# Performance work log

Measured on AMD Instinct MI355X. Metric: run time of the kernel, lower is better.

The kernel has to match this reference:

```python
import jax, jax.numpy as jnp
import numpy as np

VOL_RES = 128          # volume_res
SIGMA = 0.05           # gaussian splat sigma (normalized [0,1] coords)
SPLAT_R = 3            # splat neighborhood radius = smooth_kernel_size // 2
TET_W = 5              # tet rasterization window edge (voxels)
EPS_W = 1e-3           # weight_sum init (torch fills 0.001)

B, NV, NSURF, NF, NT = 2, 7700, 6890, 13776, 30000


def setup_inputs() -> dict:
    key = jax.random.key(0)
    k0, k1, k2, k3 = jax.random.split(key, 4)
    smpl_vertices = jax.random.uniform(k0, (B, NV, 3), dtype=jnp.float32)      # verts in [0,1]^3
    vertex_code = jax.random.uniform(k1, (B, NSURF, 3), dtype=jnp.float32)     # semantic code per surface vert
    face_indices = jax.random.randint(k2, (NF, 3), 0, NSURF, dtype=jnp.int32)
    tet_indices = jax.random.randint(k3, (NT, 4), 0, NV, dtype=jnp.int32)
    return {"smpl_vertices": smpl_vertices, "vertex_code": vertex_code,
            "face_indices": face_indices, "tet_indices": tet_indices}


def _voxelize(smpl_vertices, vertex_code, face_indices, tet_indices):
    R = VOL_RES
    R3 = R * R * R
    bsz = smpl_vertices.shape[0]

    # --- face centers / normals (computed by the torch forward; not consumed by the kernel) ---
    faces = smpl_vertices[:, face_indices]                         # (B,NF,3,3)
    face_center = faces.mean(axis=2)                               # (B,NF,3)
    v10 = faces[:, :, 0] - faces[:, :, 1]
    v12 = faces[:, :, 2] - faces[:, :, 1]
    nrm = jnp.cross(v10, v12)
    face_normal = nrm / jnp.maximum(
        jnp.linalg.norm(nrm, axis=-1, keepdims=True), 1e-5)        # F.normalize eps=1e-5
    del face_center, face_normal  # passed to the autograd fn but unused by the cuda op

    bidx = jnp.arange(bsz, dtype=jnp.int32)

    # ---------------- occupancy from tetrahedrons (point-in-tet rasterization) ----------------
    tets = smpl_vertices[:, tet_indices]                           # (B,NT,4,3)
    a = tets[:, :, 0]
    e1 = tets[:, :, 1] - a
    e2 = tets[:, :, 2] - a
    e3 = tets[:, :, 3] - a
    c23 = jnp.cross(e2, e3)
    vol6 = jnp.sum(e1 * c23, axis=-1)                              # signed 6*volume (B,NT)

    anchor = jnp.floor(jnp.min(tets, axis=2) * R).astype(jnp.int32)  # (B,NT,3) min-corner voxel
    w1 = jnp.arange(TET_W, dtype=jnp.int32)
    toff = jnp.stack(jnp.meshgrid(w1, w1, w1, indexing="ij"), -1).reshape(-1, 3)  # (W3,3) xyz
    tvox = anchor[:, :, None, :] + toff                            # (B,NT,W3,3)
    tp = (tvox.astype(jnp.float32) + 0.5) / R                      # voxel centers
    p = tp - a[:, :, None, :]                                      # (B,NT,W3,3)
    iv = 1.0 / jnp.where(jnp.abs(vol6) > 1e-12, vol6, 1.0)
    l1 = jnp.sum(p * c23[:, :, None, :], -1) * iv[:, :, None]
    l2 = jnp.sum(jnp.cross(p, e3[:, :, None, :]) * e1[:, :, None, :], -1) * iv[:, :, None]
    l3 = jnp.sum(jnp.cross(e2[:, :, None, :], p) * e1[:, :, None, :], -1) * iv[:, :, None]
    inside = (l1 >= 0) & (l2 >= 0) & (l3 >= 0) & (l1 + l2 + l3 <= 1.0)
    inside &= (jnp.abs(vol6) > 1e-12)[:, :, None]
    tvalid = jnp.all((tvox >= 0) & (tvox < R), axis=-1) & inside   # (B,NT,W3)
    # linear index, layout (b, z, y, x)
    tlin = ((bidx[:, None, None] * R + tvox[..., 2]) * R + tvox[..., 1]) * R + tvox[..., 0]
    tlin = jnp.where(tvalid, tlin, bsz * R3)                       # drop out-of-range
    occ = jnp.zeros((bsz * R3,), jnp.float32).at[tlin.reshape(-1)].max(
        tvalid.astype(jnp.float32).reshape(-1), mode="drop")

    # ---------------- gaussian semantic splat from surface vertices ----------------
    vs = smpl_vertices[:, :NSURF]                                  # (B,NS,3)
    base = jnp.floor(vs * R).astype(jnp.int32)                     # containing voxel
    o1 = jnp.arange(-SPLAT_R, SPLAT_R + 1, dtype=jnp.int32)
    offs = jnp.stack(jnp.meshgrid(o1, o1, o1, indexing="ij"), -1).reshape(-1, 3)  # (K3,3)
    svox = base[:, :, None, :] + offs                              # (B,NS,K3,3)
    ctr = (svox.astype(jnp.float32) + 0.5) / R
    d2 = jnp.sum((ctr - vs[:, :, None, :]) ** 2, axis=-1)          # (B,NS,K3)
    w = jnp.exp(-d2 / (2.0 * SIGMA * SIGMA))
    svalid = jnp.all((svox >= 0) & (svox < R), axis=-1)
    w = jnp.where(svalid, w, 0.0)
    slin = ((bidx[:, None, None] * R + svox[..., 2]) * R + svox[..., 1]) * R + svox[..., 0]
    slin = jnp.where(svalid, slin, bsz * R3).reshape(-1)

    wsum = jnp.full((bsz * R3,), EPS_W, jnp.float32).at[slin].add(w.reshape(-1), mode="drop")
    contrib = (w[..., None] * vertex_code[:, :, None, :]).reshape(-1, 3)
    sem = jnp.zeros((bsz * R3, 3), jnp.float32).at[slin].add(contrib, mode="drop")

    semantic = sem / wsum[:, None] * occ[:, None]                  # normalize + mask to body
    semantic = semantic.reshape(bsz, R, R, R, 3)                   # (B, z, y, x, C)
    return jnp.transpose(semantic, (0, 4, 1, 2, 3))                # (B, C, z, y, x)


def reference(smpl_vertices, vertex_code, face_indices, tet_indices):
    return _voxelize(smpl_vertices, vertex_code, face_indices, tet_indices)
```

## Files before the change

### kernel.cpp

```cpp
#include <hip/hip_runtime.h>
#include <math.h>

#define R 128
#define R3 (R*R*R)
#define BATCH 2
#define NV 7700
#define NSURF 6890
#define NT 30000
#define EPS_W 0.001f

#define NC 32
#define NCELLS (BATCH*NC*NC*NC)
#define CAP 12
#define SLOT_F 8
#define MAXV 128

#define BIN_TOTAL (BATCH*NSURF)
#define NT_TOTAL  (BATCH*NT)
#define TPB 256
#define TPBLK 10
#define BIN_BLOCKS ((BIN_TOTAL + TPB - 1) / TPB)
#define TET_BLOCKS ((NT_TOTAL + TPBLK - 1) / TPBLK)

__global__ __launch_bounds__(TPB) void mega_kernel(
        const float* __restrict__ verts,
        const float* __restrict__ code,
        const int*   __restrict__ tets,
        int*   __restrict__ counts,
        float* __restrict__ bins,
        unsigned char* __restrict__ occ) {
    int t = threadIdx.x;

    if (blockIdx.x < BIN_BLOCKS) {
        int idx = blockIdx.x * TPB + t;
        if (idx >= BIN_TOTAL) return;
        int v = idx % NSURF;
        int b = idx / NSURF;
        const float* vp = verts + ((size_t)b * NV + v) * 3;
        float px = vp[0], py = vp[1], pz = vp[2];
        int bx = (int)floorf(px * 128.0f);
        int by = (int)floorf(py * 128.0f);
        int bz = (int)floorf(pz * 128.0f);
        bx = min(max(bx, 0), 127); by = min(max(by, 0), 127); bz = min(max(bz, 0), 127);

        int cell = ((b * NC + (bz >> 2)) * NC + (by >> 2)) * NC + (bx >> 2);
        int slot = atomicAdd(counts + cell, 1);
        if (slot < CAP) {
            const float* cp = code + ((size_t)b * NSURF + v) * 3;
            float* s = bins + ((size_t)cell * CAP + slot) * SLOT_F;
            s[0] = px; s[1] = py; s[2] = pz;
            s[3] = cp[0]; s[4] = cp[1]; s[5] = cp[2];
        }
        return;
    }

    __shared__ float std_[TPBLK][20];
    int bt0 = (blockIdx.x - BIN_BLOCKS) * TPBLK;

    if (t < TPBLK) {
        int bt = bt0 + t;
        if (bt < NT_TOTAL) {
            int tt = bt % NT;
            int b  = bt / NT;
            int4 ti = *(const int4*)(tets + (size_t)tt * 4);
            const float* vb = verts + (size_t)b * NV * 3;

            float ax = vb[ti.x*3+0], ay = vb[ti.x*3+1], az = vb[ti.x*3+2];
            float bx = vb[ti.y*3+0], by = vb[ti.y*3+1], bz = vb[ti.y*3+2];
            float cx = vb[ti.z*3+0], cy = vb[ti.z*3+1], cz = vb[ti.z*3+2];
            float dx = vb[ti.w*3+0], dy = vb[ti.w*3+1], dz = vb[ti.w*3+2];

            float e1x = bx-ax, e1y = by-ay, e1z = bz-az;
            float e2x = cx-ax, e2y = cy-ay, e2z = cz-az;
            float e3x = dx-ax, e3y = dy-ay, e3z = dz-az;

            float c23x = e2y*e3z - e2z*e3y;
            float c23y = e2z*e3x - e2x*e3z;
            float c23z = e2x*e3y - e2y*e3x;
            float vol6 = e1x*c23x + e1y*c23y + e1z*c23z;

            int anx  = (int)floorf(fminf(fminf(ax,bx), fminf(cx,dx)) * 128.0f);
            int any_ = (int)floorf(fminf(fminf(ay,by), fminf(cy,dy)) * 128.0f);
            int anz  = (int)floorf(fminf(fminf(az,bz), fminf(cz,dz)) * 128.0f);
            int pk = (anx & 0xFF) | ((any_ & 0xFF) << 8) | ((anz & 0xFF) << 16);

            float* s = std_[t];
            s[0]=ax; s[1]=ay; s[2]=az;
            s[3]=e1x; s[4]=e1y; s[5]=e1z;
            s[6]=e2x; s[7]=e2y; s[8]=e2z;
            s[9]=e3x; s[10]=e3y; s[11]=e3z;
            s[12]=c23x; s[13]=c23y; s[14]=c23z;
            s[15]=vol6;
            s[16]=__int_as_float(pk);
        }
    }
    __syncthreads();

    if (t >= TPBLK * 25) return;
    int g = t / 25;
    int k = t % 25;
    int bt = bt0 + g;
    if (bt >= NT_TOTAL) return;
    int b = bt / NT;

    const float* s = std_[g];
    float vol6 = s[15];
    if (fabsf(vol6) <= 1e-12f) return;
    float ax = s[0],  ay = s[1],  az = s[2];
    float e1x = s[3], e1y = s[4], e1z = s[5];
    float e2x = s[6], e2y = s[7], e2z = s[8];
    float e3x = s[9], e3y = s[10], e3z = s[11];
    float c23x = s[12], c23y = s[13], c23z = s[14];
    int pk = __float_as_int(s[16]);
    int anx = pk & 0xFF, any_ = (pk >> 8) & 0xFF, anz = (pk >> 16) & 0xFF;

    int vy = any_ + k / 5;
    int vz = anz  + k % 5;
    if ((unsigned)vy >= 128u || (unsigned)vz >= 128u) return;

    const float inv = 1.0f / 128.0f;
    float iv = 1.0f / vol6;
    float py = ((float)vy + 0.5f) * inv - ay;
    float pz = ((float)vz + 0.5f) * inv - az;

    unsigned char* orow = occ + (size_t)b * R3 + ((size_t)vz * R + vy) * R;

    #pragma unroll
    for (int ddx = 0; ddx < 5; ddx++) {
        int vx = anx + ddx;
        if ((unsigned)vx >= 128u) continue;
        float px = ((float)vx + 0.5f) * inv - ax;

        float l1 = (px*c23x + py*c23y + pz*c23z) * iv;
        float cpx = py*e3z - pz*e3y;
        float cpy = pz*e3x - px*e3z;
        float cpz = px*e3y - py*e3x;
        float l2 = (cpx*e1x + cpy*e1y + cpz*e1z) * iv;
        float cqx = e2y*pz - e2z*py;
        float cqy = e2z*px - e2x*pz;
        float cqz = e2x*py - e2y*px;
        float l3 = (cqx*e1x + cqy*e1y + cqz*e1z) * iv;

        if (l1 >= 0.0f && l2 >= 0.0f && l3 >= 0.0f && (l1 + l2 + l3) <= 1.0f)
            orow[vx] = 1;
    }
}

__global__ __launch_bounds__(256) void gather_tile_kernel(
        const unsigned char* __restrict__ occ,
        const int*   __restrict__ counts,
        const float* __restrict__ bins,
        float* __restrict__ out) {
    __shared__ float4 s_a[MAXV];
    __shared__ float4 s_b[MAXV];
    __shared__ int s_n;

    int blk = blockIdx.x;
    int tx = blk & 15, ty = (blk >> 4) & 15, tz = (blk >> 8) & 15, b = blk >> 12;
    int x0 = tx << 3, y0 = ty << 3, z0 = tz << 3;

    if (threadIdx.x == 0) s_n = 0;
    __syncthreads();

    int cx0 = max(x0 - 3, 0) >> 2, cx1 = min(x0 + 10, 127) >> 2;
    int cy0 = max(y0 - 3, 0) >> 2, cy1 = min(y0 + 10, 127) >> 2;
    int cz0 = max(z0 - 3, 0) >> 2, cz1 = min(z0 + 10, 127) >> 2;
    int ncx = cx1 - cx0 + 1, ncy = cy1 - cy0 + 1, ncz = cz1 - cz0 + 1;
    int ncell = ncx * ncy * ncz;

    int t = threadIdx.x;
    if (t < ncell) {
        int lx = t % ncx; int rem = t / ncx;
        int ly = rem % ncy; int lz = rem / ncy;
        int cell = ((b * NC + cz0 + lz) * NC + cy0 + ly) * NC + cx0 + lx;
        int n = min(counts[cell], CAP);
        const float* sp = bins + (size_t)cell * CAP * SLOT_F;
        for (int j = 0; j < n; j++, sp += SLOT_F) {
            float4 A = *(const float4*)sp;
            int bx = (int)floorf(A.x * 128.0f);
            int by = (int)floorf(A.y * 128.0f);
            int bz = (int)floorf(A.z * 128.0f);
            if ((unsigned)(bx - x0 + 3) <= 13u &&
                (unsigned)(by - y0 + 3) <= 13u &&
                (unsigned)(bz - z0 + 3) <= 13u) {
                int d = atomicAdd(&s_n, 1);
                if (d < MAXV) {
                    float2 Bc = *(const float2*)(sp + 4);
                    int pk = bx | (by << 8) | (bz << 16);
                    s_a[d] = A;
                    s_b[d] = make_float4(Bc.x, Bc.y, __int_as_float(pk), 0.0f);
                }
            }
        }
    }
    __syncthreads();
    int nv = min(s_n, MAXV);

    int x = x0 + ((t & 3) << 1);
    int y = y0 + ((t >> 2) & 7);
    int z = z0 + (t >> 5);

    int L0 = (z * R + y) * R + x;
    unsigned short oc = *(const unsigned short*)(occ + (size_t)b * R3 + L0);
    int o0 = ((oc & 0xFF) == 1);
    int o1 = ((oc >> 8) == 1);

    float w0 = EPS_W, p0 = 0.0f, q0 = 0.0f, r0 = 0.0f;
    float w1 = EPS_W, p1 = 0.0f, q1 = 0.0f, r1 = 0.0f;

    if (__ballot(o0 | o1)) {
        const float inv = 1.0f / 128.0f;
        float fx0 = ((float)x + 0.5f) * inv;
        float fx1 = fx0 + inv;
        float fy  = ((float)y + 0.5f) * inv;
        float fz  = ((float)z + 0.5f) * inv;
        for (int j = 0; j < nv; j++) {
            float4 A  = s_a[j];
            float4 Bv = s_b[j];
            int pk = __float_as_int(Bv.z);
            int bx = pk & 0xFF, by = (pk >> 8) & 0xFF, bz = (pk >> 16) & 0xFF;
            if ((unsigned)(y - by + 3) <= 6u && (unsigned)(z - bz + 3) <= 6u) {
                float ddy = fy - A.y, ddz = fz - A.z;
                float dyz = ddy*ddy + ddz*ddz;
                int dx0 = x - bx;
                if ((unsigned)(dx0 + 3) <= 6u) {
                    float ddx = fx0 - A.x;
                    float w = __expf(-200.0f * (ddx*ddx + dyz));
                    w0 += w; p0 += w*A.w; q0 += w*Bv.x; r0 += w*Bv.y;
                }
                if ((unsigned)(dx0 + 4) <= 6u) {
                    float ddx = fx1 - A.x;
                    float w = __expf(-200.0f * (ddx*ddx + dyz));
                    w1 += w; p1 += w*A.w; q1 += w*Bv.x; r1 += w*Bv.y;
                }
            }
        }
    }
    float s0 = o0 ? 1.0f / w0 : 0.0f;
    float s1 = o1 ? 1.0f / w1 : 0.0f;
    float* ob = out + (size_t)b * 3 * R3 + L0;
    *(float2*)(ob)        = make_float2(p0 * s0, p1 * s1);
    *(float2*)(ob + R3)   = make_float2(q0 * s0, q1 * s1);
    *(float2*)(ob + 2*R3) = make_float2(r0 * s0, r1 * s1);
}

extern "C" void kernel_launch(void* const* d_in, const int* in_sizes, int n_in,
                              void* d_out, int out_size, void* d_ws, size_t ws_size,
                              hipStream_t stream) {
    const float* smpl_vertices = (const float*)d_in[0];
    const float* vertex_code   = (const float*)d_in[1];
    const int*   tet_indices   = (const int*)d_in[3];
    float* out = (float*)d_out;

    unsigned char* occ = (unsigned char*)d_ws;
    int*   counts = (int*)(occ + (size_t)BATCH * R3);
    float* bins   = (float*)(counts + NCELLS);

    hipMemsetAsync(counts, 0, (size_t)NCELLS * sizeof(int), stream);

    mega_kernel<<<BIN_BLOCKS + TET_BLOCKS, TPB, 0, stream>>>(
        smpl_vertices, vertex_code, tet_indices, counts, bins, occ);

    const int ntiles = BATCH * 16 * 16 * 16;
    gather_tile_kernel<<<ntiles, 256, 0, stream>>>(occ, counts, bins, out);
}
```

Baseline: 108.4 us.

## Split gather tiles into per-wavefront 8x4x4 subtiles with private candidate lists

```diff
diff --git a/kernel.cpp b/kernel.cpp
--- a/kernel.cpp
+++ b/kernel.cpp
@@ -13,7 +13,7 @@
 #define NCELLS (BATCH*NC*NC*NC)
 #define CAP 12
 #define SLOT_F 8
-#define MAXV 128
+#define GT_MAXV 64
 
 #define BIN_TOTAL (BATCH*NSURF)
 #define NT_TOTAL  (BATCH*NT)
@@ -151,26 +151,29 @@
         const int*   __restrict__ counts,
         const float* __restrict__ bins,
         float* __restrict__ out) {
-    __shared__ float4 s_a[MAXV];
-    __shared__ float4 s_b[MAXV];
-    __shared__ int s_n;
-
-    int blk = blockIdx.x;
-    int tx = blk & 15, ty = (blk >> 4) & 15, tz = (blk >> 8) & 15, b = blk >> 12;
-    int x0 = tx << 3, y0 = ty << 3, z0 = tz << 3;
-
-    if (threadIdx.x == 0) s_n = 0;
+    __shared__ float4 s_a[4][GT_MAXV];
+    __shared__ float4 s_b[4][GT_MAXV];
+    __shared__ int s_n[4];
+
+    int t = threadIdx.x;
+    int w = t >> 6;
+    int lane = t & 63;
+
+    int tile = blockIdx.x * 4 + w;
+    int tx = tile & 15, ty = (tile >> 4) & 31, tz = (tile >> 9) & 31, b = tile >> 14;
+    int x0 = tx << 3, y0 = ty << 2, z0 = tz << 2;
+
+    if (lane == 0) s_n[w] = 0;
     __syncthreads();
 
     int cx0 = max(x0 - 3, 0) >> 2, cx1 = min(x0 + 10, 127) >> 2;
-    int cy0 = max(y0 - 3, 0) >> 2, cy1 = min(y0 + 10, 127) >> 2;
-    int cz0 = max(z0 - 3, 0) >> 2, cz1 = min(z0 + 10, 127) >> 2;
+    int cy0 = max(y0 - 3, 0) >> 2, cy1 = min(y0 + 6, 127) >> 2;
+    int cz0 = max(z0 - 3, 0) >> 2, cz1 = min(z0 + 6, 127) >> 2;
     int ncx = cx1 - cx0 + 1, ncy = cy1 - cy0 + 1, ncz = cz1 - cz0 + 1;
     int ncell = ncx * ncy * ncz;
 
-    int t = threadIdx.x;
-    if (t < ncell) {
-        int lx = t % ncx; int rem = t / ncx;
+    if (lane < ncell) {
+        int lx = lane % ncx; int rem = lane / ncx;
         int ly = rem % ncy; int lz = rem / ncy;
         int cell = ((b * NC + cz0 + lz) * NC + cy0 + ly) * NC + cx0 + lx;
         int n = min(counts[cell], CAP);
@@ -181,24 +184,24 @@
             int by = (int)floorf(A.y * 128.0f);
             int bz = (int)floorf(A.z * 128.0f);
             if ((unsigned)(bx - x0 + 3) <= 13u &&
-                (unsigned)(by - y0 + 3) <= 13u &&
-                (unsigned)(bz - z0 + 3) <= 13u) {
-                int d = atomicAdd(&s_n, 1);
-                if (d < MAXV) {
+                (unsigned)(by - y0 + 3) <= 9u &&
+                (unsigned)(bz - z0 + 3) <= 9u) {
+                int d = atomicAdd(&s_n[w], 1);
+                if (d < GT_MAXV) {
                     float2 Bc = *(const float2*)(sp + 4);
                     int pk = bx | (by << 8) | (bz << 16);
-                    s_a[d] = A;
-                    s_b[d] = make_float4(Bc.x, Bc.y, __int_as_float(pk), 0.0f);
+                    s_a[w][d] = A;
+                    s_b[w][d] = make_float4(Bc.x, Bc.y, __int_as_float(pk), 0.0f);
                 }
             }
         }
     }
     __syncthreads();
-    int nv = min(s_n, MAXV);
-
-    int x = x0 + ((t & 3) << 1);
-    int y = y0 + ((t >> 2) & 7);
-    int z = z0 + (t >> 5);
+    int nv = min(s_n[w], GT_MAXV);
+
+    int x = x0 + ((lane & 3) << 1);
+    int y = y0 + ((lane >> 2) & 3);
+    int z = z0 + (lane >> 4);
 
     int L0 = (z * R + y) * R + x;
     unsigned short oc = *(const unsigned short*)(occ + (size_t)b * R3 + L0);
@@ -215,8 +218,8 @@
         float fy  = ((float)y + 0.5f) * inv;
         float fz  = ((float)z + 0.5f) * inv;
         for (int j = 0; j < nv; j++) {
-            float4 A  = s_a[j];
-            float4 Bv = s_b[j];
+            float4 A  = s_a[w][j];
+            float4 Bv = s_b[w][j];
             int pk = __float_as_int(Bv.z);
             int bx = pk & 0xFF, by = (pk >> 8) & 0xFF, bz = (pk >> 16) & 0xFF;
             if ((unsigned)(y - by + 3) <= 6u && (unsigned)(z - bz + 3) <= 6u) {
@@ -225,13 +228,13 @@
                 int dx0 = x - bx;
                 if ((unsigned)(dx0 + 3) <= 6u) {
                     float ddx = fx0 - A.x;
-                    float w = __expf(-200.0f * (ddx*ddx + dyz));
-                    w0 += w; p0 += w*A.w; q0 += w*Bv.x; r0 += w*Bv.y;
+                    float ww = __expf(-200.0f * (ddx*ddx + dyz));
+                    w0 += ww; p0 += ww*A.w; q0 += ww*Bv.x; r0 += ww*Bv.y;
                 }
                 if ((unsigned)(dx0 + 4) <= 6u) {
                     float ddx = fx1 - A.x;
-                    float w = __expf(-200.0f * (ddx*ddx + dyz));
-                    w1 += w; p1 += w*A.w; q1 += w*Bv.x; r1 += w*Bv.y;
+                    float ww = __expf(-200.0f * (ddx*ddx + dyz));
+                    w1 += ww; p1 += ww*A.w; q1 += ww*Bv.x; r1 += ww*Bv.y;
                 }
             }
         }
@@ -261,6 +264,5 @@
     mega_kernel<<<BIN_BLOCKS + TET_BLOCKS, TPB, 0, stream>>>(
         smpl_vertices, vertex_code, tet_indices, counts, bins, occ);
 
-    const int ntiles = BATCH * 16 * 16 * 16;
-    gather_tile_kernel<<<ntiles, 256, 0, stream>>>(occ, counts, bins, out);
+    gather_tile_kernel<<<8192, 256, 0, stream>>>(occ, counts, bins, out);
 }
```

New measurement: 100.4 us. -7.4%, faster.
